# Kernel tuning notes

Measured on AMD Instinct MI355X. Metric: run time of the kernel, lower is better.

The kernel has to match this reference:

```python
import jax, jax.numpy as jnp
import numpy as np

HEADS = 16
D_MODEL = 1024
D_HEAD = D_MODEL // HEADS


def setup_inputs() -> dict:
    key = jax.random.key(0)
    ks = jax.random.split(key, 9)
    s_h = 1.0 / np.sqrt(D_HEAD)
    s_m = 1.0 / np.sqrt(D_MODEL)
    return {
        "x": jax.random.normal(ks[0], (4, 2048, D_MODEL), dtype=jnp.float32),
        "Wq": jax.random.uniform(ks[1], (D_HEAD, D_HEAD), jnp.float32, -s_h, s_h),
        "bq": jax.random.uniform(ks[2], (D_HEAD,), jnp.float32, -s_h, s_h),
        "Wk": jax.random.uniform(ks[3], (D_HEAD, D_HEAD), jnp.float32, -s_h, s_h),
        "bk": jax.random.uniform(ks[4], (D_HEAD,), jnp.float32, -s_h, s_h),
        "Wv": jax.random.uniform(ks[5], (D_HEAD, D_HEAD), jnp.float32, -s_h, s_h),
        "bv": jax.random.uniform(ks[6], (D_HEAD,), jnp.float32, -s_h, s_h),
        "Wp": jax.random.uniform(ks[7], (D_MODEL, D_MODEL), jnp.float32, -s_m, s_m),
        "bp": jax.random.uniform(ks[8], (D_MODEL,), jnp.float32, -s_m, s_m),
    }


def reference(x, Wq, bq, Wk, bk, Wv, bv, Wp, bp):
    B, T, C = x.shape
    xh = x.reshape(B, T, HEADS, D_HEAD)  # [B,T,H,Dh]
    # per-head linear projections (torch Linear: x @ W.T + b)
    q = jnp.einsum('bthd,ed->bhte', xh, Wq) + bq  # [B,H,T,Dh]
    k = jnp.einsum('bthd,ed->bhte', xh, Wk) + bk
    v = jnp.einsum('bthd,ed->bhte', xh, Wv) + bv
    # NOTE: original scales by sqrt(C) = sqrt(d_model), not sqrt(d_head)
    att = jnp.einsum('bhqd,bhkd->bhqk', q, k) / jnp.sqrt(jnp.float32(C))
    att = jax.nn.softmax(att, axis=-1)
    out = jnp.einsum('bhqk,bhkd->bhqd', att, v)  # [B,H,T,Dh]
    out = out.transpose(0, 2, 1, 3).reshape(B, T, C)
    return out @ Wp.T + bp
```

## Files before the change

kernel.cpp:

```cpp
#include <hip/hip_runtime.h>
#include <hip/hip_bf16.h>
#include <cstddef>

#define B_  4
#define T_  2048
#define H_  16
#define DH  64
#define C_  1024
#define BH  64

typedef float  f32x16 __attribute__((ext_vector_type(16)));
typedef __bf16 bf16x8 __attribute__((ext_vector_type(8)));
typedef __bf16 bf16x4 __attribute__((ext_vector_type(4)));

#define MFMA32(a, b, c) __builtin_amdgcn_mfma_f32_32x32x16_bf16(a, b, c, 0, 0, 0)


__device__ __forceinline__ unsigned cvt_pk_bf16(float lo, float hi) {
    unsigned r;
    asm("v_cvt_pk_bf16_f32 %0, %1, %2" : "=v"(r) : "v"(lo), "v"(hi));
    return r;
}

__global__ __launch_bounds__(256) void qkv_kernel(
    const float* __restrict__ x,
    const float* __restrict__ Wq, const float* __restrict__ bq,
    const float* __restrict__ Wk, const float* __restrict__ bk,
    const float* __restrict__ Wv, const float* __restrict__ bv,
    __bf16* __restrict__ q, __bf16* __restrict__ kf, __bf16* __restrict__ vf,
    const float* __restrict__ Wp, __bf16* __restrict__ wpf)
{
    __shared__ __bf16 Xs[128 * 72];
    __shared__ __bf16 Ws[3][64 * 72];
    __bf16* Vtl = Xs;
    __bf16* Kst = &Ws[0][0];

    const int tt  = blockIdx.x;
    const int bh  = blockIdx.y;
    const int b   = bh >> 4, h = bh & 15;
    const int t0  = tt * 128;
    const int tid = threadIdx.x;
    const int wave = tid >> 6, lane = tid & 63;
    const int m = lane & 31, hh = lane >> 5;

    #pragma unroll
    for (int i = 0; i < 8; ++i) {
        const int idx = i * 256 + tid;
        const int r = idx >> 4, c = (idx & 15) * 4;
        const float4 x4 = *(const float4*)(x + ((size_t)(b * T_ + t0 + r)) * C_ + h * DH + c);
        const unsigned lo = ((unsigned)__builtin_bit_cast(unsigned short, (__bf16)x4.y) << 16)
                          | (unsigned)__builtin_bit_cast(unsigned short, (__bf16)x4.x);
        const unsigned hi = ((unsigned)__builtin_bit_cast(unsigned short, (__bf16)x4.w) << 16)
                          | (unsigned)__builtin_bit_cast(unsigned short, (__bf16)x4.z);
        *(unsigned*)&Xs[r * 72 + c]     = lo;
        *(unsigned*)&Xs[r * 72 + c + 2] = hi;
    }
    #pragma unroll
    for (int i = 0; i < 4; ++i) {
        const int idx = i * 256 + tid;
        const int r = idx >> 4, c = (idx & 15) * 4;
        const float* wsrc[3] = {Wq, Wk, Wv};
        #pragma unroll
        for (int wv_ = 0; wv_ < 3; ++wv_) {
            const float4 w4 = *(const float4*)(wsrc[wv_] + r * 64 + c);
            const unsigned lo = ((unsigned)__builtin_bit_cast(unsigned short, (__bf16)w4.y) << 16)
                              | (unsigned)__builtin_bit_cast(unsigned short, (__bf16)w4.x);
            const unsigned hi = ((unsigned)__builtin_bit_cast(unsigned short, (__bf16)w4.w) << 16)
                              | (unsigned)__builtin_bit_cast(unsigned short, (__bf16)w4.z);
            *(unsigned*)&Ws[wv_][r * 72 + c]     = lo;
            *(unsigned*)&Ws[wv_][r * 72 + c + 2] = hi;
        }
    }
    __syncthreads();

    bf16x8 xf[4];
    #pragma unroll
    for (int ks = 0; ks < 4; ++ks)
        xf[ks] = *(const bf16x8*)&Xs[(wave * 32 + m) * 72 + ks * 16 + hh * 8];
    __syncthreads();

    const float s32 = 0.03125f * 1.4426950408889634f;

    unsigned kpk[16];

    #pragma unroll
    for (int mat = 0; mat < 3; ++mat) {
        f32x16 acc0 = {}, acc1 = {};
        #pragma unroll
        for (int ks = 0; ks < 4; ++ks) {
            const bf16x8 w0 = *(const bf16x8*)&Ws[mat][(m) * 72 + ks * 16 + hh * 8];
            const bf16x8 w1 = *(const bf16x8*)&Ws[mat][(32 + m) * 72 + ks * 16 + hh * 8];
            acc0 = MFMA32(xf[ks], w0, acc0);
            acc1 = MFMA32(xf[ks], w1, acc1);
        }
        const float* bias = (mat == 0) ? bq : (mat == 1) ? bk : bv;
        const float b0 = bias[m], b1 = bias[32 + m];
        #pragma unroll
        for (int r = 0; r < 16; ++r) {
            const int R = (r & 3) + 8 * (r >> 2) + 4 * hh;
            const int tloc = wave * 32 + R;
            const float v0 = acc0[r] + b0, v1 = acc1[r] + b1;
            if (mat == 0) {
                const size_t base = ((size_t)bh * T_ + t0 + tloc) * DH;
                q[base + m]      = (__bf16)(v0 * s32);
                q[base + 32 + m] = (__bf16)(v1 * s32);
            } else if (mat == 1) {
                kpk[r] = ((unsigned)__builtin_bit_cast(unsigned short, (__bf16)v1) << 16)
                       |  (unsigned)__builtin_bit_cast(unsigned short, (__bf16)v0);
            } else {
                Vtl[(m) * 136 + tloc]      = (__bf16)v0;
                Vtl[(32 + m) * 136 + tloc] = (__bf16)v1;
            }
        }
    }
    __syncthreads();

    #pragma unroll
    for (int r = 0; r < 16; ++r) {
        const int R = (r & 3) + 8 * (r >> 2) + 4 * hh;
        const int tloc = wave * 32 + R;
        Kst[tloc * 72 + m]      = __builtin_bit_cast(__bf16, (unsigned short)(kpk[r] & 0xffff));
        Kst[tloc * 72 + 32 + m] = __builtin_bit_cast(__bf16, (unsigned short)(kpk[r] >> 16));
    }

    #pragma unroll
    for (int i = 0; i < 4; ++i) {
        const int idx = i * 256 + tid;
        const int ln = idx & 63, c_ = idx >> 6;
        const int kt64l = c_ >> 3, dh = (c_ >> 2) & 1, cN = c_ & 3;
        const __bf16* src = &Vtl[(dh * 32 + (ln & 31)) * 136 + kt64l * 64 + cN * 16 + (ln >> 5) * 8];
        __bf16* dst = vf + ((((size_t)(bh * 32 + tt * 2 + kt64l) * 2 + dh) * 4 + cN) * 64 + ln) * 8;
        *(uint4*)dst = *(const uint4*)src;
    }
    __syncthreads();

    #pragma unroll
    for (int i = 0; i < 4; ++i) {
        const int idx = i * 256 + tid;
        const int ln = idx & 63, c_ = idx >> 6;
        const int kt64l = c_ >> 3, rh = (c_ >> 2) & 1, ks = c_ & 3;
        const __bf16* src = &Kst[(kt64l * 64 + rh * 32 + (ln & 31)) * 72 + ks * 16 + (ln >> 5) * 8];
        __bf16* dst = kf + ((((size_t)(bh * 32 + tt * 2 + kt64l) * 2 + rh) * 4 + ks) * 64 + ln) * 8;
        *(uint4*)dst = *(const uint4*)src;
    }

    if (wpf != nullptr && tid < 128) {
        const int ci = (bh * 16 + tt) * 128 + tid;
        const int ln = ci & 63;
        const int ks = (ci >> 6) & 3;
        const int n  = (ci >> 8) & 3;
        const int cb = (ci >> 10) & 15;
        const int eb = ci >> 14;
        const int row = eb * 128 + n * 32 + (ln & 31);
        const int col = cb * 64 + ks * 16 + (ln >> 5) * 8;
        const float4 w0 = *(const float4*)(Wp + (size_t)row * C_ + col);
        const float4 w1 = *(const float4*)(Wp + (size_t)row * C_ + col + 4);
        uint4 p;
        p.x = ((unsigned)__builtin_bit_cast(unsigned short, (__bf16)w0.y) << 16)
            |  (unsigned)__builtin_bit_cast(unsigned short, (__bf16)w0.x);
        p.y = ((unsigned)__builtin_bit_cast(unsigned short, (__bf16)w0.w) << 16)
            |  (unsigned)__builtin_bit_cast(unsigned short, (__bf16)w0.z);
        p.z = ((unsigned)__builtin_bit_cast(unsigned short, (__bf16)w1.y) << 16)
            |  (unsigned)__builtin_bit_cast(unsigned short, (__bf16)w1.x);
        p.w = ((unsigned)__builtin_bit_cast(unsigned short, (__bf16)w1.w) << 16)
            |  (unsigned)__builtin_bit_cast(unsigned short, (__bf16)w1.z);
        *(uint4*)(wpf + (size_t)ci * 8) = p;
    }
}

__global__ __launch_bounds__(256, 2) void attn_kernel(
    const __bf16* __restrict__ q, const __bf16* __restrict__ kf,
    const __bf16* __restrict__ vf, __bf16* __restrict__ af)
{
    const int bh  = blockIdx.x;
    const int q0  = blockIdx.y * 256;
    const int tid = threadIdx.x;
    const int wave = tid >> 6, lane = tid & 63;
    const int m = lane & 31, h = lane >> 5;
    const int row0 = q0 + wave * 64;

    const __bf16* qb  = q  + (size_t)bh * T_ * DH;
    const __bf16* kfb = kf + (size_t)bh * (T_ * DH);
    const __bf16* vfb = vf + (size_t)bh * (T_ * DH);

    bf16x8 qfa[4], qfb_[4];
    #pragma unroll
    for (int ks = 0; ks < 4; ++ks) {
        qfa[ks]  = *(const bf16x8*)(qb + (size_t)(row0 + m) * DH + ks * 16 + h * 8);
        qfb_[ks] = *(const bf16x8*)(qb + (size_t)(row0 + 32 + m) * DH + ks * 16 + h * 8);
    }

    f32x16 Oa0 = {}, Oa1 = {}, Ob0 = {}, Ob1 = {};
    float lsa = 0.f, lsb = 0.f;

    for (int kt = 0; kt < 32; ++kt) {
        const __bf16* kt_k = kfb + kt * 4096;
        const __bf16* kt_v = vfb + kt * 4096;
        #pragma unroll
        for (int rh = 0; rh < 2; ++rh) {
            bf16x8 kfr[4];
            #pragma unroll
            for (int ks = 0; ks < 4; ++ks)
                kfr[ks] = *(const bf16x8*)(kt_k + rh * 2048 + ks * 512 + lane * 8);
            f32x16 Sa = {}, Sb = {};
            #pragma unroll
            for (int ks = 0; ks < 4; ++ks) {
                Sa = MFMA32(kfr[ks], qfa[ks],  Sa);
                Sb = MFMA32(kfr[ks], qfb_[ks], Sb);
            }

            #pragma unroll
            for (int cc = 0; cc < 2; ++cc) {
                const int rb = cc * 8;
                float a0f = __builtin_amdgcn_exp2f(Sa[rb + 0]);
                float a1f = __builtin_amdgcn_exp2f(Sa[rb + 1]);
                float a2f = __builtin_amdgcn_exp2f(Sa[rb + 2]);
                float a3f = __builtin_amdgcn_exp2f(Sa[rb + 3]);
                float a4f = __builtin_amdgcn_exp2f(Sa[rb + 4]);
                float a5f = __builtin_amdgcn_exp2f(Sa[rb + 5]);
                float a6f = __builtin_amdgcn_exp2f(Sa[rb + 6]);
                float a7f = __builtin_amdgcn_exp2f(Sa[rb + 7]);
                lsa += ((a0f + a1f) + (a2f + a3f)) + ((a4f + a5f) + (a6f + a7f));
                unsigned pa0 = cvt_pk_bf16(a0f, a1f);
                unsigned pa1 = cvt_pk_bf16(a2f, a3f);
                unsigned pa2 = cvt_pk_bf16(a4f, a5f);
                unsigned pa3 = cvt_pk_bf16(a6f, a7f);
                asm("v_permlane32_swap_b32 %0, %1" : "+v"(pa0), "+v"(pa2));
                asm("v_permlane32_swap_b32 %0, %1" : "+v"(pa1), "+v"(pa3));
                const uint4 pwa = {pa0, pa1, pa2, pa3};
                const bf16x8 pba = __builtin_bit_cast(bf16x8, pwa);
                float b0f = __builtin_amdgcn_exp2f(Sb[rb + 0]);
                float b1f = __builtin_amdgcn_exp2f(Sb[rb + 1]);
                float b2f = __builtin_amdgcn_exp2f(Sb[rb + 2]);
                float b3f = __builtin_amdgcn_exp2f(Sb[rb + 3]);
                float b4f = __builtin_amdgcn_exp2f(Sb[rb + 4]);
                float b5f = __builtin_amdgcn_exp2f(Sb[rb + 5]);
                float b6f = __builtin_amdgcn_exp2f(Sb[rb + 6]);
                float b7f = __builtin_amdgcn_exp2f(Sb[rb + 7]);
                lsb += ((b0f + b1f) + (b2f + b3f)) + ((b4f + b5f) + (b6f + b7f));
                unsigned pb0 = cvt_pk_bf16(b0f, b1f);
                unsigned pb1 = cvt_pk_bf16(b2f, b3f);
                unsigned pb2 = cvt_pk_bf16(b4f, b5f);
                unsigned pb3 = cvt_pk_bf16(b6f, b7f);
                asm("v_permlane32_swap_b32 %0, %1" : "+v"(pb0), "+v"(pb2));
                asm("v_permlane32_swap_b32 %0, %1" : "+v"(pb1), "+v"(pb3));
                const uint4 pwb = {pb0, pb1, pb2, pb3};
                const bf16x8 pbb = __builtin_bit_cast(bf16x8, pwb);

                const int c = rh * 2 + cc;
                const bf16x8 v0 = *(const bf16x8*)(kt_v + c * 512 + lane * 8);
                const bf16x8 v1 = *(const bf16x8*)(kt_v + 2048 + c * 512 + lane * 8);
                Oa0 = MFMA32(v0, pba, Oa0);
                Oa1 = MFMA32(v1, pba, Oa1);
                Ob0 = MFMA32(v0, pbb, Ob0);
                Ob1 = MFMA32(v1, pbb, Ob1);
            }
        }
    }

    lsa += __shfl_xor(lsa, 32);
    lsb += __shfl_xor(lsb, 32);
    const float linva = 1.0f / lsa, linvb = 1.0f / lsb;

    const int qt = row0 >> 7;
    const int wv_a = (row0 >> 5) & 3;
    __bf16* ab_a = af + ((size_t)(bh * 16 + qt)) * 8192 + wv_a * 2048 + lane * 8;
    __bf16* ab_b = ab_a + 2048;
    #pragma unroll
    for (int ks = 0; ks < 4; ++ks) {
        {
            const f32x16& Og = (ks < 2) ? Oa0 : Oa1;
            const int rb = (ks & 1) * 8;
            unsigned a0 = cvt_pk_bf16(Og[rb + 0] * linva, Og[rb + 1] * linva);
            unsigned a1 = cvt_pk_bf16(Og[rb + 2] * linva, Og[rb + 3] * linva);
            unsigned b0 = cvt_pk_bf16(Og[rb + 4] * linva, Og[rb + 5] * linva);
            unsigned b1 = cvt_pk_bf16(Og[rb + 6] * linva, Og[rb + 7] * linva);
            asm("v_permlane32_swap_b32 %0, %1" : "+v"(a0), "+v"(b0));
            asm("v_permlane32_swap_b32 %0, %1" : "+v"(a1), "+v"(b1));
            const uint4 pw = {a0, a1, b0, b1};
            *(uint4*)(ab_a + ks * 512) = pw;
        }
        {
            const f32x16& Og = (ks < 2) ? Ob0 : Ob1;
            const int rb = (ks & 1) * 8;
            unsigned a0 = cvt_pk_bf16(Og[rb + 0] * linvb, Og[rb + 1] * linvb);
            unsigned a1 = cvt_pk_bf16(Og[rb + 2] * linvb, Og[rb + 3] * linvb);
            unsigned b0 = cvt_pk_bf16(Og[rb + 4] * linvb, Og[rb + 5] * linvb);
            unsigned b1 = cvt_pk_bf16(Og[rb + 6] * linvb, Og[rb + 7] * linvb);
            asm("v_permlane32_swap_b32 %0, %1" : "+v"(a0), "+v"(b0));
            asm("v_permlane32_swap_b32 %0, %1" : "+v"(a1), "+v"(b1));
            const uint4 pw = {a0, a1, b0, b1};
            *(uint4*)(ab_b + ks * 512) = pw;
        }
    }
}

__global__ __launch_bounds__(256) void wpconv_kernel(
    const float* __restrict__ Wp, __bf16* __restrict__ wpf)
{
    const int ci = blockIdx.x * 256 + threadIdx.x;
    const int ln = ci & 63;
    const int ks = (ci >> 6) & 3;
    const int n  = (ci >> 8) & 3;
    const int cb = (ci >> 10) & 15;
    const int eb = ci >> 14;
    const int row = eb * 128 + n * 32 + (ln & 31);
    const int col = cb * 64 + ks * 16 + (ln >> 5) * 8;
    const float4 w0 = *(const float4*)(Wp + (size_t)row * C_ + col);
    const float4 w1 = *(const float4*)(Wp + (size_t)row * C_ + col + 4);
    uint4 p;
    p.x = ((unsigned)__builtin_bit_cast(unsigned short, (__bf16)w0.y) << 16)
        |  (unsigned)__builtin_bit_cast(unsigned short, (__bf16)w0.x);
    p.y = ((unsigned)__builtin_bit_cast(unsigned short, (__bf16)w0.w) << 16)
        |  (unsigned)__builtin_bit_cast(unsigned short, (__bf16)w0.z);
    p.z = ((unsigned)__builtin_bit_cast(unsigned short, (__bf16)w1.y) << 16)
        |  (unsigned)__builtin_bit_cast(unsigned short, (__bf16)w1.x);
    p.w = ((unsigned)__builtin_bit_cast(unsigned short, (__bf16)w1.w) << 16)
        |  (unsigned)__builtin_bit_cast(unsigned short, (__bf16)w1.z);
    *(uint4*)(wpf + (size_t)ci * 8) = p;
}

__global__ __launch_bounds__(256) void proj_kernel(
    const __bf16* __restrict__ af,
    const __bf16* __restrict__ wpf,
    const float* __restrict__ bp,
    float* __restrict__ out)
{
    const int tb2 = blockIdx.x, eb = blockIdx.y;
    const int tid = threadIdx.x;
    const int wave = tid >> 6, lane = tid & 63;
    const int m = lane & 31, h = lane >> 5;
    const int b = tb2 >> 5, rem = tb2 & 31;
    const int qtile = rem >> 1, half = rem & 1;
    const int wv = half * 2 + (wave & 1);
    const int eh = wave >> 1;
    const int e0 = eb * 128;

    const __bf16* abase = af + ((size_t)(b * 256 + qtile)) * 8192
                             + wv * 2048 + lane * 8;
    const __bf16* wbase = wpf + (size_t)eb * 131072 + eh * 4096 + lane * 8;

    f32x16 acc[2] = {f32x16{}, f32x16{}};

    for (int cb = 0; cb < 16; ++cb) {
        const __bf16* ap = abase + (size_t)cb * 131072;
        const __bf16* wp = wbase + (size_t)cb * 8192;
        bf16x8 afr[4];
        #pragma unroll
        for (int ks = 0; ks < 4; ++ks)
            afr[ks] = *(const bf16x8*)(ap + ks * 512);
        #pragma unroll
        for (int n = 0; n < 2; ++n) {
            #pragma unroll
            for (int ks = 0; ks < 4; ++ks) {
                const bf16x8 bf = *(const bf16x8*)(wp + (n * 4 + ks) * 512);
                acc[n] = MFMA32(afr[ks], bf, acc[n]);
            }
        }
    }

    const int tokbase = b * T_ + qtile * 128 + wv * 32;
    #pragma unroll
    for (int n = 0; n < 2; ++n) {
        const int e = e0 + (eh * 2 + n) * 32 + m;
        const float bias = bp[e];
        #pragma unroll
        for (int r = 0; r < 16; ++r) {
            const int R = (r & 3) + 8 * (r >> 2) + 4 * h;
            out[(size_t)(tokbase + R) * C_ + e] = acc[n][r] + bias;
        }
    }
}

extern "C" void kernel_launch(void* const* d_in, const int* in_sizes, int n_in,
                              void* d_out, int out_size, void* d_ws, size_t ws_size,
                              hipStream_t stream)
{
    const float* x  = (const float*)d_in[0];
    const float* Wq = (const float*)d_in[1];
    const float* bq = (const float*)d_in[2];
    const float* Wk = (const float*)d_in[3];
    const float* bk = (const float*)d_in[4];
    const float* Wv = (const float*)d_in[5];
    const float* bv = (const float*)d_in[6];
    const float* Wp = (const float*)d_in[7];
    const float* bp = (const float*)d_in[8];

    const size_t N = (size_t)BH * T_ * DH;
    __bf16* qws  = (__bf16*)d_ws;
    __bf16* kws  = qws + N;
    __bf16* vtws = kws + N;
    __bf16* aws  = vtws + N;

    const size_t need = 4 * N * sizeof(__bf16) + (size_t)C_ * C_ * sizeof(__bf16);
    const bool roomy = ws_size >= need;
    __bf16* wpf = roomy ? (aws + N) : qws;

    qkv_kernel<<<dim3(16, 64), 256, 0, stream>>>(
        x, Wq, bq, Wk, bk, Wv, bv, qws, kws, vtws,
        Wp, roomy ? wpf : nullptr);
    attn_kernel<<<dim3(64, 8), 256, 0, stream>>>(qws, kws, vtws, aws);
    if (!roomy)
        wpconv_kernel<<<dim3(512), 256, 0, stream>>>(Wp, wpf);
    proj_kernel<<<dim3(128, 8), 256, 0, stream>>>(aws, wpf, bp, (float*)d_out);
}
```

Baseline: 225.8 us.

## Emit Q/K/V directly in MFMA fragment layout and enlarge projection tiles

```diff
diff --git a/kernel.cpp b/kernel.cpp
--- a/kernel.cpp
+++ b/kernel.cpp
@@ -11,7 +11,6 @@
 
 typedef float  f32x16 __attribute__((ext_vector_type(16)));
 typedef __bf16 bf16x8 __attribute__((ext_vector_type(8)));
-typedef __bf16 bf16x4 __attribute__((ext_vector_type(4)));
 
 #define MFMA32(a, b, c) __builtin_amdgcn_mfma_f32_32x32x16_bf16(a, b, c, 0, 0, 0)
 
@@ -20,6 +19,17 @@
     unsigned r;
     asm("v_cvt_pk_bf16_f32 %0, %1, %2" : "=v"(r) : "v"(lo), "v"(hi));
     return r;
+}
+
+__device__ __forceinline__ uint4 frag_pack(const f32x16& Og, int rb, float s) {
+    unsigned a0 = cvt_pk_bf16(Og[rb + 0] * s, Og[rb + 1] * s);
+    unsigned a1 = cvt_pk_bf16(Og[rb + 2] * s, Og[rb + 3] * s);
+    unsigned b0 = cvt_pk_bf16(Og[rb + 4] * s, Og[rb + 5] * s);
+    unsigned b1 = cvt_pk_bf16(Og[rb + 6] * s, Og[rb + 7] * s);
+    asm("v_permlane32_swap_b32 %0, %1" : "+v"(a0), "+v"(b0));
+    asm("v_permlane32_swap_b32 %0, %1" : "+v"(a1), "+v"(b1));
+    uint4 pw; pw.x = a0; pw.y = a1; pw.z = b0; pw.w = b1;
+    return pw;
 }
 
 __global__ __launch_bounds__(256) void qkv_kernel(
@@ -27,13 +37,11 @@
     const float* __restrict__ Wq, const float* __restrict__ bq,
     const float* __restrict__ Wk, const float* __restrict__ bk,
     const float* __restrict__ Wv, const float* __restrict__ bv,
-    __bf16* __restrict__ q, __bf16* __restrict__ kf, __bf16* __restrict__ vf,
+    __bf16* __restrict__ qf, __bf16* __restrict__ kf, __bf16* __restrict__ vf,
     const float* __restrict__ Wp, __bf16* __restrict__ wpf)
 {
     __shared__ __bf16 Xs[128 * 72];
     __shared__ __bf16 Ws[3][64 * 72];
-    __bf16* Vtl = Xs;
-    __bf16* Kst = &Ws[0][0];
 
     const int tt  = blockIdx.x;
     const int bh  = blockIdx.y;
@@ -77,71 +85,62 @@
     #pragma unroll
     for (int ks = 0; ks < 4; ++ks)
         xf[ks] = *(const bf16x8*)&Xs[(wave * 32 + m) * 72 + ks * 16 + hh * 8];
-    __syncthreads();
 
     const float s32 = 0.03125f * 1.4426950408889634f;
-
-    unsigned kpk[16];
-
-    #pragma unroll
-    for (int mat = 0; mat < 3; ++mat) {
+    const int kt64l = wave >> 1, rh = wave & 1;
+
+    #pragma unroll
+    for (int mat = 0; mat < 2; ++mat) {
         f32x16 acc0 = {}, acc1 = {};
         #pragma unroll
         for (int ks = 0; ks < 4; ++ks) {
             const bf16x8 w0 = *(const bf16x8*)&Ws[mat][(m) * 72 + ks * 16 + hh * 8];
             const bf16x8 w1 = *(const bf16x8*)&Ws[mat][(32 + m) * 72 + ks * 16 + hh * 8];
+            acc0 = MFMA32(w0, xf[ks], acc0);
+            acc1 = MFMA32(w1, xf[ks], acc1);
+        }
+        const float* bias = (mat == 0) ? bq : bk;
+        #pragma unroll
+        for (int g = 0; g < 4; ++g) {
+            const float4 bA = *(const float4*)(bias + 4 * hh + 8 * g);
+            const float4 bB = *(const float4*)(bias + 32 + 4 * hh + 8 * g);
+            acc0[4*g+0] += bA.x; acc0[4*g+1] += bA.y;
+            acc0[4*g+2] += bA.z; acc0[4*g+3] += bA.w;
+            acc1[4*g+0] += bB.x; acc1[4*g+1] += bB.y;
+            acc1[4*g+2] += bB.z; acc1[4*g+3] += bB.w;
+        }
+        const float sc = (mat == 0) ? s32 : 1.0f;
+        __bf16* base = (mat == 0)
+            ? qf + ((size_t)(bh * 16 + tt)) * 8192 + wave * 2048 + lane * 8
+            : kf + (((size_t)(bh * 32 + tt * 2 + kt64l) * 2 + rh) * 4) * 512 + lane * 8;
+        #pragma unroll
+        for (int ks = 0; ks < 4; ++ks) {
+            const f32x16& Og = (ks < 2) ? acc0 : acc1;
+            *(uint4*)(base + ks * 512) = frag_pack(Og, (ks & 1) * 8, sc);
+        }
+    }
+
+    {
+        f32x16 acc0 = {}, acc1 = {};
+        #pragma unroll
+        for (int ks = 0; ks < 4; ++ks) {
+            const bf16x8 w0 = *(const bf16x8*)&Ws[2][(m) * 72 + ks * 16 + hh * 8];
+            const bf16x8 w1 = *(const bf16x8*)&Ws[2][(32 + m) * 72 + ks * 16 + hh * 8];
             acc0 = MFMA32(xf[ks], w0, acc0);
             acc1 = MFMA32(xf[ks], w1, acc1);
         }
-        const float* bias = (mat == 0) ? bq : (mat == 1) ? bk : bv;
-        const float b0 = bias[m], b1 = bias[32 + m];
-        #pragma unroll
-        for (int r = 0; r < 16; ++r) {
-            const int R = (r & 3) + 8 * (r >> 2) + 4 * hh;
-            const int tloc = wave * 32 + R;
-            const float v0 = acc0[r] + b0, v1 = acc1[r] + b1;
-            if (mat == 0) {
-                const size_t base = ((size_t)bh * T_ + t0 + tloc) * DH;
-                q[base + m]      = (__bf16)(v0 * s32);
-                q[base + 32 + m] = (__bf16)(v1 * s32);
-            } else if (mat == 1) {
-                kpk[r] = ((unsigned)__builtin_bit_cast(unsigned short, (__bf16)v1) << 16)
-                       |  (unsigned)__builtin_bit_cast(unsigned short, (__bf16)v0);
-            } else {
-                Vtl[(m) * 136 + tloc]      = (__bf16)v0;
-                Vtl[(32 + m) * 136 + tloc] = (__bf16)v1;
-            }
-        }
-    }
-    __syncthreads();
-
-    #pragma unroll
-    for (int r = 0; r < 16; ++r) {
-        const int R = (r & 3) + 8 * (r >> 2) + 4 * hh;
-        const int tloc = wave * 32 + R;
-        Kst[tloc * 72 + m]      = __builtin_bit_cast(__bf16, (unsigned short)(kpk[r] & 0xffff));
-        Kst[tloc * 72 + 32 + m] = __builtin_bit_cast(__bf16, (unsigned short)(kpk[r] >> 16));
-    }
-
-    #pragma unroll
-    for (int i = 0; i < 4; ++i) {
-        const int idx = i * 256 + tid;
-        const int ln = idx & 63, c_ = idx >> 6;
-        const int kt64l = c_ >> 3, dh = (c_ >> 2) & 1, cN = c_ & 3;
-        const __bf16* src = &Vtl[(dh * 32 + (ln & 31)) * 136 + kt64l * 64 + cN * 16 + (ln >> 5) * 8];
-        __bf16* dst = vf + ((((size_t)(bh * 32 + tt * 2 + kt64l) * 2 + dh) * 4 + cN) * 64 + ln) * 8;
-        *(uint4*)dst = *(const uint4*)src;
-    }
-    __syncthreads();
-
-    #pragma unroll
-    for (int i = 0; i < 4; ++i) {
-        const int idx = i * 256 + tid;
-        const int ln = idx & 63, c_ = idx >> 6;
-        const int kt64l = c_ >> 3, rh = (c_ >> 2) & 1, ks = c_ & 3;
-        const __bf16* src = &Kst[(kt64l * 64 + rh * 32 + (ln & 31)) * 72 + ks * 16 + (ln >> 5) * 8];
-        __bf16* dst = kf + ((((size_t)(bh * 32 + tt * 2 + kt64l) * 2 + rh) * 4 + ks) * 64 + ln) * 8;
-        *(uint4*)dst = *(const uint4*)src;
+        const float b0v = bv[m], b1v = bv[32 + m];
+        #pragma unroll
+        for (int r = 0; r < 16; ++r) { acc0[r] += b0v; acc1[r] += b1v; }
+        __bf16* vbase = vf + (((size_t)(bh * 32 + tt * 2 + kt64l) * 2) * 4) * 512 + lane * 8;
+        #pragma unroll
+        for (int dh = 0; dh < 2; ++dh) {
+            const f32x16& Og = dh ? acc1 : acc0;
+            #pragma unroll
+            for (int cl = 0; cl < 2; ++cl)
+                *(uint4*)(vbase + dh * 2048 + (rh * 2 + cl) * 512)
+                    = frag_pack(Og, cl * 8, 1.0f);
+        }
     }
 
     if (wpf != nullptr && tid < 128) {
@@ -169,7 +168,7 @@
 }
 
 __global__ __launch_bounds__(256, 2) void attn_kernel(
-    const __bf16* __restrict__ q, const __bf16* __restrict__ kf,
+    const __bf16* __restrict__ qf, const __bf16* __restrict__ kf,
     const __bf16* __restrict__ vf, __bf16* __restrict__ af)
 {
     const int bh  = blockIdx.x;
@@ -179,15 +178,16 @@
     const int m = lane & 31, h = lane >> 5;
     const int row0 = q0 + wave * 64;
 
-    const __bf16* qb  = q  + (size_t)bh * T_ * DH;
     const __bf16* kfb = kf + (size_t)bh * (T_ * DH);
     const __bf16* vfb = vf + (size_t)bh * (T_ * DH);
 
+    const __bf16* qbase = qf + ((size_t)(bh * 16 + (row0 >> 7))) * 8192
+                             + ((row0 >> 5) & 3) * 2048 + lane * 8;
     bf16x8 qfa[4], qfb_[4];
     #pragma unroll
     for (int ks = 0; ks < 4; ++ks) {
-        qfa[ks]  = *(const bf16x8*)(qb + (size_t)(row0 + m) * DH + ks * 16 + h * 8);
-        qfb_[ks] = *(const bf16x8*)(qb + (size_t)(row0 + 32 + m) * DH + ks * 16 + h * 8);
+        qfa[ks]  = *(const bf16x8*)(qbase + ks * 512);
+        qfb_[ks] = *(const bf16x8*)(qbase + 2048 + ks * 512);
     }
 
     f32x16 Oa0 = {}, Oa1 = {}, Ob0 = {}, Ob1 = {};
@@ -268,30 +268,8 @@
     __bf16* ab_b = ab_a + 2048;
     #pragma unroll
     for (int ks = 0; ks < 4; ++ks) {
-        {
-            const f32x16& Og = (ks < 2) ? Oa0 : Oa1;
-            const int rb = (ks & 1) * 8;
-            unsigned a0 = cvt_pk_bf16(Og[rb + 0] * linva, Og[rb + 1] * linva);
-            unsigned a1 = cvt_pk_bf16(Og[rb + 2] * linva, Og[rb + 3] * linva);
-            unsigned b0 = cvt_pk_bf16(Og[rb + 4] * linva, Og[rb + 5] * linva);
-            unsigned b1 = cvt_pk_bf16(Og[rb + 6] * linva, Og[rb + 7] * linva);
-            asm("v_permlane32_swap_b32 %0, %1" : "+v"(a0), "+v"(b0));
-            asm("v_permlane32_swap_b32 %0, %1" : "+v"(a1), "+v"(b1));
-            const uint4 pw = {a0, a1, b0, b1};
-            *(uint4*)(ab_a + ks * 512) = pw;
-        }
-        {
-            const f32x16& Og = (ks < 2) ? Ob0 : Ob1;
-            const int rb = (ks & 1) * 8;
-            unsigned a0 = cvt_pk_bf16(Og[rb + 0] * linvb, Og[rb + 1] * linvb);
-            unsigned a1 = cvt_pk_bf16(Og[rb + 2] * linvb, Og[rb + 3] * linvb);
-            unsigned b0 = cvt_pk_bf16(Og[rb + 4] * linvb, Og[rb + 5] * linvb);
-            unsigned b1 = cvt_pk_bf16(Og[rb + 6] * linvb, Og[rb + 7] * linvb);
-            asm("v_permlane32_swap_b32 %0, %1" : "+v"(a0), "+v"(b0));
-            asm("v_permlane32_swap_b32 %0, %1" : "+v"(a1), "+v"(b1));
-            const uint4 pw = {a0, a1, b0, b1};
-            *(uint4*)(ab_b + ks * 512) = pw;
-        }
+        *(uint4*)(ab_a + ks * 512) = frag_pack((ks < 2) ? Oa0 : Oa1, (ks & 1) * 8, linva);
+        *(uint4*)(ab_b + ks * 512) = frag_pack((ks < 2) ? Ob0 : Ob1, (ks & 1) * 8, linvb);
     }
 }
 
@@ -326,48 +304,54 @@
     const float* __restrict__ bp,
     float* __restrict__ out)
 {
-    const int tb2 = blockIdx.x, eb = blockIdx.y;
+    const int tb = blockIdx.x, eb = blockIdx.y;
     const int tid = threadIdx.x;
     const int wave = tid >> 6, lane = tid & 63;
     const int m = lane & 31, h = lane >> 5;
-    const int b = tb2 >> 5, rem = tb2 & 31;
-    const int qtile = rem >> 1, half = rem & 1;
-    const int wv = half * 2 + (wave & 1);
-    const int eh = wave >> 1;
+    const int b = tb >> 3;
+    const int qt = (tb & 7) * 2 + (wave >> 1);
+    const int wv0 = (wave & 1) * 2;
     const int e0 = eb * 128;
 
-    const __bf16* abase = af + ((size_t)(b * 256 + qtile)) * 8192
-                             + wv * 2048 + lane * 8;
-    const __bf16* wbase = wpf + (size_t)eb * 131072 + eh * 4096 + lane * 8;
-
-    f32x16 acc[2] = {f32x16{}, f32x16{}};
+    const __bf16* abase = af + ((size_t)(b * 256 + qt)) * 8192
+                             + wv0 * 2048 + lane * 8;
+    const __bf16* wbase = wpf + (size_t)eb * 131072 + lane * 8;
+
+    f32x16 acc[2][4] = {};
 
     for (int cb = 0; cb < 16; ++cb) {
         const __bf16* ap = abase + (size_t)cb * 131072;
         const __bf16* wp = wbase + (size_t)cb * 8192;
-        bf16x8 afr[4];
-        #pragma unroll
-        for (int ks = 0; ks < 4; ++ks)
-            afr[ks] = *(const bf16x8*)(ap + ks * 512);
-        #pragma unroll
-        for (int n = 0; n < 2; ++n) {
+        bf16x8 a0[4], a1[4];
+        #pragma unroll
+        for (int ks = 0; ks < 4; ++ks) {
+            a0[ks] = *(const bf16x8*)(ap + ks * 512);
+            a1[ks] = *(const bf16x8*)(ap + 2048 + ks * 512);
+        }
+        #pragma unroll
+        for (int n = 0; n < 4; ++n) {
             #pragma unroll
             for (int ks = 0; ks < 4; ++ks) {
                 const bf16x8 bf = *(const bf16x8*)(wp + (n * 4 + ks) * 512);
-                acc[n] = MFMA32(afr[ks], bf, acc[n]);
+                acc[0][n] = MFMA32(a0[ks], bf, acc[0][n]);
+                acc[1][n] = MFMA32(a1[ks], bf, acc[1][n]);
             }
         }
     }
 
-    const int tokbase = b * T_ + qtile * 128 + wv * 32;
-    #pragma unroll
-    for (int n = 0; n < 2; ++n) {
-        const int e = e0 + (eh * 2 + n) * 32 + m;
+    const int tokb = b * T_ + qt * 128;
+    #pragma unroll
+    for (int n = 0; n < 4; ++n) {
+        const int e = e0 + n * 32 + m;
         const float bias = bp[e];
         #pragma unroll
-        for (int r = 0; r < 16; ++r) {
-            const int R = (r & 3) + 8 * (r >> 2) + 4 * h;
-            out[(size_t)(tokbase + R) * C_ + e] = acc[n][r] + bias;
+        for (int u = 0; u < 2; ++u) {
+            const int t0 = tokb + (wv0 + u) * 32;
+            #pragma unroll
+            for (int r = 0; r < 16; ++r) {
+                const int R = (r & 3) + 8 * (r >> 2) + 4 * h;
+                out[(size_t)(t0 + R) * C_ + e] = acc[u][n][r] + bias;
+            }
         }
     }
 }
@@ -402,5 +386,5 @@
     attn_kernel<<<dim3(64, 8), 256, 0, stream>>>(qws, kws, vtws, aws);
     if (!roomy)
         wpconv_kernel<<<dim3(512), 256, 0, stream>>>(Wp, wpf);
-    proj_kernel<<<dim3(128, 8), 256, 0, stream>>>(aws, wpf, bp, (float*)d_out);
-}
+    proj_kernel<<<dim3(32, 8), 256, 0, stream>>>(aws, wpf, bp, (float*)d_out);
+}
```

Result: no change. 222.2 us (-1.6%).
